# Kernel optimization log

Measured on AMD Instinct MI355X. Metric: run time of the kernel, lower is better.

Reference implementation:

```python
import jax, jax.numpy as jnp
import numpy as np

B, N, K, D, L = 32, 1024, 16, 256, 256


def setup_inputs() -> dict:
    key = jax.random.key(0)
    k1, k2, k3, k4 = jax.random.split(key, 4)
    targets = jax.random.normal(k1, (B, N, D), dtype=jnp.float32)
    neighbors = jax.random.normal(k2, (B, N, K, D), dtype=jnp.float32)
    a = jax.random.uniform(k3, (B, N, K + 1), dtype=jnp.float32)
    # glorot-uniform-ish kernel
    limit = np.sqrt(6.0 / (D + L)).astype(np.float32)
    kernel = jax.random.uniform(k4, (D, L), dtype=jnp.float32, minval=-limit, maxval=limit)
    return {"targets": targets, "neighbors": neighbors, "a": a, "kernel": kernel}


def reference(targets, neighbors, a, kernel):
    # neighborhood: [B, N, K+1, D] = self node prepended to its K neighbors
    neighborhood = jnp.concatenate([targets[..., None, :], neighbors], axis=-2)
    # matmul with kernel then sum over neighborhood axis (fused via einsum)
    y = jnp.einsum("bnkd,dl->bnl", neighborhood, kernel)  # [B, N, L]
    # degree normalization; guard against isolated nodes (degree ~ 0)
    factor = jnp.sum(a, axis=-1, keepdims=True)  # [B, N, 1]
    factor = jnp.where(factor > 0.5, factor, jnp.ones_like(factor))
    y = y / factor
    # dropout is a no-op at inference; use_bias=False
    return jax.nn.relu(y)
```

## Files before the change

kernel.cpp:

```cpp
#include <hip/hip_runtime.h>


typedef float v4f __attribute__((ext_vector_type(4)));

#define BB 32
#define NN 1024
#define KK 16
#define DD 256
#define LL 256
#define ROWS 32
#define DTILE 16
#define NTHREADS 256

__global__ __launch_bounds__(NTHREADS, 3)
void gcn_fused(const float* __restrict__ targets,
               const float* __restrict__ neighbors,
               const float* __restrict__ a,
               const float* __restrict__ kern,
               float* __restrict__ out) {
    __shared__ float s[ROWS * DD];
    __shared__ float kt[DTILE * LL];
    __shared__ float invf[ROWS];

    const int t        = threadIdx.x;
    const int w        = t >> 6;
    const int lane     = t & 63;
    const int row_base = blockIdx.x * ROWS;

    if (t < ROWS) {
        const float* ap = a + (row_base + t) * (KK + 1);
        float f = 0.0f;
        #pragma unroll
        for (int j = 0; j < KK + 1; ++j) f += ap[j];
        invf[t] = (f > 0.5f) ? (1.0f / f) : 1.0f;
    }

    const v4f* t4 = (const v4f*)targets;
    const v4f* n4 = (const v4f*)neighbors;
    #pragma unroll
    for (int r = 0; r < 8; ++r) {
        const int rl   = w * 8 + r;
        const int grow = row_base + rl;
        v4f accum = __builtin_nontemporal_load(&t4[grow * (DD / 4) + lane]);
        #pragma unroll
        for (int k = 0; k < KK; ++k) {
            accum += __builtin_nontemporal_load(&n4[(grow * KK + k) * (DD / 4) + lane]);
        }
        *(v4f*)&s[rl * DD + lane * 4] = accum;
    }

    v4f acc[8];
    #pragma unroll
    for (int r = 0; r < 8; ++r) acc[r] = v4f{0.0f, 0.0f, 0.0f, 0.0f};

    const v4f* k4 = (const v4f*)kern;
    for (int dt = 0; dt < DD / DTILE; ++dt) {
        __syncthreads();
        #pragma unroll
        for (int i = 0; i < (DTILE * LL / 4) / NTHREADS; ++i) {
            v4f v = k4[dt * (DTILE * LL / 4) + i * NTHREADS + t];
            *(v4f*)&kt[(i * NTHREADS + t) * 4] = v;
        }
        __syncthreads();
        #pragma unroll
        for (int dd = 0; dd < DTILE / 4; ++dd) {
            const int d0 = dt * DTILE + dd * 4;
            v4f kv0 = *(const v4f*)&kt[(dd * 4 + 0) * LL + lane * 4];
            v4f kv1 = *(const v4f*)&kt[(dd * 4 + 1) * LL + lane * 4];
            v4f kv2 = *(const v4f*)&kt[(dd * 4 + 2) * LL + lane * 4];
            v4f kv3 = *(const v4f*)&kt[(dd * 4 + 3) * LL + lane * 4];
            #pragma unroll
            for (int r = 0; r < 8; ++r) {
                v4f sv = *(const v4f*)&s[(w * 8 + r) * DD + d0];
                acc[r] += sv.x * kv0;
                acc[r] += sv.y * kv1;
                acc[r] += sv.z * kv2;
                acc[r] += sv.w * kv3;
            }
        }
    }

    #pragma unroll
    for (int r = 0; r < 8; ++r) {
        const int rl  = w * 8 + r;
        const float inv = invf[rl];
        v4f v = acc[r] * inv;
        v.x = fmaxf(v.x, 0.0f);
        v.y = fmaxf(v.y, 0.0f);
        v.z = fmaxf(v.z, 0.0f);
        v.w = fmaxf(v.w, 0.0f);
        __builtin_nontemporal_store(v, (v4f*)&out[(row_base + rl) * LL + lane * 4]);
    }
}

extern "C" void kernel_launch(void* const* d_in, const int* in_sizes, int n_in,
                              void* d_out, int out_size, void* d_ws, size_t ws_size,
                              hipStream_t stream) {
    const float* targets   = (const float*)d_in[0];
    const float* neighbors = (const float*)d_in[1];
    const float* a         = (const float*)d_in[2];
    const float* kern      = (const float*)d_in[3];
    float* out = (float*)d_out;
    const int blocks = (BB * NN) / ROWS;
    gcn_fused<<<dim3(blocks), dim3(NTHREADS), 0, stream>>>(targets, neighbors, a, kern, out);
}
```

Measured before the change: 738.5 us.

## Keep aggregated rows in registers and double-buffer kernel tiles via readlane broadcast

Result: no change. 730.7 us (-1.1%).

```diff
diff --git a/kernel.cpp b/kernel.cpp
--- a/kernel.cpp
+++ b/kernel.cpp
@@ -10,16 +10,20 @@
 #define LL 256
 #define ROWS 32
 #define DTILE 16
+#define NPASS (DD / DTILE)
 #define NTHREADS 256
 
-__global__ __launch_bounds__(NTHREADS, 3)
+__device__ __forceinline__ float bcast_lane(float x, int lane) {
+    return __int_as_float(__builtin_amdgcn_readlane(__float_as_int(x), lane));
+}
+
+__global__ __launch_bounds__(NTHREADS, 4)
 void gcn_fused(const float* __restrict__ targets,
                const float* __restrict__ neighbors,
                const float* __restrict__ a,
                const float* __restrict__ kern,
                float* __restrict__ out) {
-    __shared__ float s[ROWS * DD];
-    __shared__ float kt[DTILE * LL];
+    __shared__ float kt[2][DTILE * LL];
     __shared__ float invf[ROWS];
 
     const int t        = threadIdx.x;
@@ -27,8 +31,14 @@
     const int lane     = t & 63;
     const int row_base = blockIdx.x * ROWS;
 
+    const v4f* k4 = (const v4f*)kern;
+
+    v4f stage[4];
+    #pragma unroll
+    for (int i = 0; i < 4; ++i) stage[i] = k4[i * NTHREADS + t];
+
     if (t < ROWS) {
-        const float* ap = a + (row_base + t) * (KK + 1);
+        const float* ap = a + (size_t)(row_base + t) * (KK + 1);
         float f = 0.0f;
         #pragma unroll
         for (int j = 0; j < KK + 1; ++j) f += ap[j];
@@ -37,59 +47,64 @@
 
     const v4f* t4 = (const v4f*)targets;
     const v4f* n4 = (const v4f*)neighbors;
+    v4f sreg[8];
     #pragma unroll
     for (int r = 0; r < 8; ++r) {
-        const int rl   = w * 8 + r;
-        const int grow = row_base + rl;
-        v4f accum = __builtin_nontemporal_load(&t4[grow * (DD / 4) + lane]);
-        #pragma unroll
+        const int grow = row_base + w * 8 + r;
+        v4f accum = __builtin_nontemporal_load(&t4[(size_t)grow * (DD / 4) + lane]);
+        #pragma unroll 4
         for (int k = 0; k < KK; ++k) {
-            accum += __builtin_nontemporal_load(&n4[(grow * KK + k) * (DD / 4) + lane]);
+            accum += __builtin_nontemporal_load(
+                &n4[((size_t)grow * KK + k) * (DD / 4) + lane]);
         }
-        *(v4f*)&s[rl * DD + lane * 4] = accum;
+        sreg[r] = accum;
     }
+
+    #pragma unroll
+    for (int i = 0; i < 4; ++i)
+        *(v4f*)&kt[0][(i * NTHREADS + t) * 4] = stage[i];
+    __syncthreads();
 
     v4f acc[8];
     #pragma unroll
     for (int r = 0; r < 8; ++r) acc[r] = v4f{0.0f, 0.0f, 0.0f, 0.0f};
 
-    const v4f* k4 = (const v4f*)kern;
-    for (int dt = 0; dt < DD / DTILE; ++dt) {
-        __syncthreads();
+    for (int dt = 0; dt < NPASS; ++dt) {
+        const int cur = dt & 1;
+        if (dt < NPASS - 1) {
+            #pragma unroll
+            for (int i = 0; i < 4; ++i)
+                stage[i] = k4[(dt + 1) * (DTILE * LL / 4) + i * NTHREADS + t];
+        }
         #pragma unroll
-        for (int i = 0; i < (DTILE * LL / 4) / NTHREADS; ++i) {
-            v4f v = k4[dt * (DTILE * LL / 4) + i * NTHREADS + t];
-            *(v4f*)&kt[(i * NTHREADS + t) * 4] = v;
-        }
-        __syncthreads();
-        #pragma unroll
-        for (int dd = 0; dd < DTILE / 4; ++dd) {
-            const int d0 = dt * DTILE + dd * 4;
-            v4f kv0 = *(const v4f*)&kt[(dd * 4 + 0) * LL + lane * 4];
-            v4f kv1 = *(const v4f*)&kt[(dd * 4 + 1) * LL + lane * 4];
-            v4f kv2 = *(const v4f*)&kt[(dd * 4 + 2) * LL + lane * 4];
-            v4f kv3 = *(const v4f*)&kt[(dd * 4 + 3) * LL + lane * 4];
+        for (int dd = 0; dd < DTILE; ++dd) {
+            v4f kv = *(const v4f*)&kt[cur][dd * LL + 4 * lane];
+            const int chunk = dt * (DTILE / 4) + (dd >> 2);
             #pragma unroll
             for (int r = 0; r < 8; ++r) {
-                v4f sv = *(const v4f*)&s[(w * 8 + r) * DD + d0];
-                acc[r] += sv.x * kv0;
-                acc[r] += sv.y * kv1;
-                acc[r] += sv.z * kv2;
-                acc[r] += sv.w * kv3;
+                const float sv = bcast_lane(sreg[r][dd & 3], chunk);
+                acc[r] += sv * kv;
             }
+        }
+        if (dt < NPASS - 1) {
+            *(v4f*)&kt[cur ^ 1][(0 * NTHREADS + t) * 4] = stage[0];
+            *(v4f*)&kt[cur ^ 1][(1 * NTHREADS + t) * 4] = stage[1];
+            *(v4f*)&kt[cur ^ 1][(2 * NTHREADS + t) * 4] = stage[2];
+            *(v4f*)&kt[cur ^ 1][(3 * NTHREADS + t) * 4] = stage[3];
+            __syncthreads();
         }
     }
 
     #pragma unroll
     for (int r = 0; r < 8; ++r) {
-        const int rl  = w * 8 + r;
+        const int rl    = w * 8 + r;
         const float inv = invf[rl];
         v4f v = acc[r] * inv;
         v.x = fmaxf(v.x, 0.0f);
         v.y = fmaxf(v.y, 0.0f);
         v.z = fmaxf(v.z, 0.0f);
         v.w = fmaxf(v.w, 0.0f);
-        __builtin_nontemporal_store(v, (v4f*)&out[(row_base + rl) * LL + lane * 4]);
+        __builtin_nontemporal_store(v, (v4f*)&out[(size_t)(row_base + rl) * LL + 4 * lane]);
     }
 }
 
```
